# Kernel tuning notes

Hardware: AMD Instinct MI355X
Metric: run time of the kernel (lower is better)

## Reference

```python
import jax, jax.numpy as jnp
import numpy as np

QUANT_BLOCK = 32  # GGUF Q4_0-style block size
QUANT_ZERO = 8.0  # 4-bit codes are offset-binary around 8


def setup_inputs() -> dict:
    key = jax.random.key(0)
    k_x, k_q, k_s, k_up, k_dn, k_b = jax.random.split(key, 6)
    O, I, R = 4096, 4096, 16
    T = 2048  # tokens (batch*seq)
    x = jax.random.normal(k_x, (T, I), dtype=jnp.float32)
    # quantized 4-bit codes stored unpacked as int32 in [0, 16)
    q = jax.random.randint(k_q, (O, I), 0, 16, dtype=jnp.int32)
    # per-block scales (small positive, like real GGUF d values)
    scales = jax.random.uniform(k_s, (O, I // QUANT_BLOCK), dtype=jnp.float32) * 0.05
    lora_up = jax.random.normal(k_up, (O, R), dtype=jnp.float32) * 0.02
    lora_down = jax.random.normal(k_dn, (R, I), dtype=jnp.float32) * 0.02
    alpha = jnp.ones((), dtype=jnp.float32)
    bias = jax.random.normal(k_b, (O,), dtype=jnp.float32)
    return {"x": x, "q": q, "scales": scales, "lora_up": lora_up,
            "lora_down": lora_down, "alpha": alpha, "bias": bias}


def _dequant(q, scales):
    # q: [O, I] int codes; scales: [O, I/BLOCK] per-block scale
    O, I = q.shape
    qf = q.reshape(O, I // QUANT_BLOCK, QUANT_BLOCK).astype(scales.dtype)
    w = (qf - QUANT_ZERO) * scales[:, :, None]  # [O, I/B, B]
    return w.reshape(O, I)


def reference(x, q, scales, lora_up, lora_down, alpha, bias):
    # on-the-fly dequant (GGMLLayer.get_weight -> dequantize_tensor)
    W = _dequant(q, scales)  # [O, I]
    # LoRA patch apply (ray_calculate_weight): W += alpha * up @ down
    W = W + alpha * jnp.einsum('or,ri->oi', lora_up, lora_down)
    # linear forward: y = x @ W^T + b
    return jnp.einsum('ti,oi->to', x, W) + bias
```

## Files before the change

kernel.cpp:

```cpp
#include <hip/hip_runtime.h>
#include <hip/hip_bf16.h>
#include <stdint.h>

#define T_DIM 2048
#define I_DIM 4096
#define O_DIM 4096
#define R_DIM 16
#define QBLK  32

typedef __bf16 bf16x8 __attribute__((ext_vector_type(8)));
typedef float  floatx4 __attribute__((ext_vector_type(4)));
typedef unsigned short ushort_t;

#define AS1 __attribute__((address_space(1)))
#define AS3 __attribute__((address_space(3)))

__device__ __forceinline__ ushort_t f2bf(float f) {
  unsigned u = __float_as_uint(f);
  u += 0x7FFFu + ((u >> 16) & 1u);
  return (ushort_t)(u >> 16);
}

__device__ __forceinline__ float dot4(float4 a, float4 b) {
  return a.x * b.x + a.y * b.y + a.z * b.z + a.w * b.w;
}

__global__ __launch_bounds__(256) void k_prep(const float* __restrict__ x,
                                              const int* __restrict__ q,
                                              const float* __restrict__ scales,
                                              const float* __restrict__ down,
                                              const float* __restrict__ alphap,
                                              ushort_t* __restrict__ xb,
                                              ushort_t* __restrict__ wb,
                                              float* __restrict__ xd) {
  __shared__ float ds[16 * 512];
  const int b = blockIdx.x, tid = threadIdx.x;

  if (b < 4096) {
    int idx = b * 256 + tid;
    const float4* xp = (const float4*)x;
    float4 a = xp[idx * 2], c = xp[idx * 2 + 1];
    union { ushort_t u[8]; uint4 v; } r;
    r.u[0] = f2bf(a.x); r.u[1] = f2bf(a.y); r.u[2] = f2bf(a.z); r.u[3] = f2bf(a.w);
    r.u[4] = f2bf(c.x); r.u[5] = f2bf(c.y); r.u[6] = f2bf(c.z); r.u[7] = f2bf(c.w);
    ((uint4*)xb)[idx] = r.v;
    return;
  }
  if (b < 12288) {
    int idx = (b - 4096) * 256 + tid;
    int o  = idx >> 9;
    int i0 = (idx & 511) * 8;
    float s = scales[o * (I_DIM / QBLK) + (i0 >> 5)];
    const int4* qp = (const int4*)(q + (size_t)o * I_DIM + i0);
    int4 q0 = qp[0], q1 = qp[1];
    union { ushort_t u[8]; uint4 v; } r;
    r.u[0] = f2bf((float)(q0.x - 8) * s); r.u[1] = f2bf((float)(q0.y - 8) * s);
    r.u[2] = f2bf((float)(q0.z - 8) * s); r.u[3] = f2bf((float)(q0.w - 8) * s);
    r.u[4] = f2bf((float)(q1.x - 8) * s); r.u[5] = f2bf((float)(q1.y - 8) * s);
    r.u[6] = f2bf((float)(q1.z - 8) * s); r.u[7] = f2bf((float)(q1.w - 8) * s);
    ((uint4*)wb)[idx] = r.v;
    return;
  }
  {
    const int blk = b - 12288;
    const int tl = tid >> 5, s = tid & 31;
    const int t = blk * 8 + tl;
    float acc[16];
#pragma unroll
    for (int r = 0; r < 16; ++r) acc[r] = 0.f;
    for (int c = 0; c < 8; ++c) {
      const int ib = c * 512;
      __syncthreads();
#pragma unroll
      for (int j = 0; j < 8; ++j) {
        int e = j * 256 + tid;
        int r = e >> 7, col = e & 127;
        ((float4*)ds)[e] = ((const float4*)(down + (size_t)r * I_DIM + ib))[col];
      }
      __syncthreads();
#pragma unroll
      for (int j = 0; j < 4; ++j) {
        float4 xv = ((const float4*)(x + (size_t)t * I_DIM + ib))[s + 32 * j];
#pragma unroll
        for (int r = 0; r < 16; ++r) {
          float4 dv = ((const float4*)ds)[r * 128 + s + 32 * j];
          acc[r] += dot4(xv, dv);
        }
      }
    }
    const float al = alphap[0];
#pragma unroll
    for (int r = 0; r < 16; ++r) {
      float v = acc[r];
      v += __shfl_down(v, 16, 32);
      v += __shfl_down(v, 8, 32);
      v += __shfl_down(v, 4, 32);
      v += __shfl_down(v, 2, 32);
      v += __shfl_down(v, 1, 32);
      if (s == 0) xd[t * 16 + r] = v * al;
    }
  }
}


#define BK 32
#define NT (I_DIM / BK)
#define TILE_E (128 * BK)

__device__ __forceinline__ void stage2(const ushort_t* __restrict__ g,
                                       ushort_t* lds0, int wv, int lane) {
#pragma unroll
  for (int it = 0; it < 2; ++it) {
    const int seg_base = it * 256 + wv * 64;
    const int seg = seg_base + lane;
    const int r  = seg >> 2;
    const int cg = (seg & 3) ^ (r & 3);
    __builtin_amdgcn_global_load_lds(
        (const AS1 char*)(g + (size_t)r * I_DIM + cg * 8),
        (AS3 char*)(lds0 + seg_base * 8), 16, 0, 0);
  }
}

template<int VM, bool STG>
__device__ __forceinline__ void ktile(const ushort_t* __restrict__ Ac,
                                      const ushort_t* __restrict__ Bc,
                                      ushort_t* Ast, ushort_t* Bst,
                                      const ushort_t* ga, const ushort_t* gb,
                                      floatx4 (&acc)[4][4], int wv, int lane) {
  const int quad = lane >> 4, m16 = lane & 15;
  const int wm = wv >> 1, wn = wv & 1;
  bf16x8 af[4], bf0[2], bf1[2];

#pragma unroll
  for (int im = 0; im < 4; ++im) {
    const int m = wm * 64 + im * 16 + m16;
    af[im] = *(const bf16x8*)(Ac + (m * 4 + (quad ^ (m & 3))) * 8);
  }
#pragma unroll
  for (int in_ = 0; in_ < 2; ++in_) {
    const int n = wn * 64 + in_ * 16 + m16;
    bf0[in_] = *(const bf16x8*)(Bc + (n * 4 + (quad ^ (n & 3))) * 8);
  }
  if constexpr (STG) stage2(ga, Ast, wv, lane);
  __builtin_amdgcn_s_barrier();
  asm volatile("s_waitcnt lgkmcnt(0)" ::: "memory");
  __builtin_amdgcn_sched_barrier(0);
  __builtin_amdgcn_s_setprio(1);
#pragma unroll
  for (int im = 0; im < 4; ++im)
#pragma unroll
    for (int in_ = 0; in_ < 2; ++in_)
      acc[im][in_] = __builtin_amdgcn_mfma_f32_16x16x32_bf16(
          af[im], bf0[in_], acc[im][in_], 0, 0, 0);
  __builtin_amdgcn_s_setprio(0);
  __builtin_amdgcn_s_barrier();

#pragma unroll
  for (int in_ = 0; in_ < 2; ++in_) {
    const int n = wn * 64 + (in_ + 2) * 16 + m16;
    bf1[in_] = *(const bf16x8*)(Bc + (n * 4 + (quad ^ (n & 3))) * 8);
  }
  if constexpr (STG) stage2(gb, Bst, wv, lane);
  __builtin_amdgcn_s_barrier();
  asm volatile("s_waitcnt lgkmcnt(0)" ::: "memory");
  __builtin_amdgcn_sched_barrier(0);
  __builtin_amdgcn_s_setprio(1);
#pragma unroll
  for (int im = 0; im < 4; ++im)
#pragma unroll
    for (int in_ = 0; in_ < 2; ++in_)
      acc[im][in_ + 2] = __builtin_amdgcn_mfma_f32_16x16x32_bf16(
          af[im], bf1[in_], acc[im][in_ + 2], 0, 0, 0);
  __builtin_amdgcn_s_setprio(0);
  if constexpr (VM == 8)      asm volatile("s_waitcnt vmcnt(8)" ::: "memory");
  else if constexpr (VM == 4) asm volatile("s_waitcnt vmcnt(4)" ::: "memory");
  else if constexpr (VM == 0) asm volatile("s_waitcnt vmcnt(0)" ::: "memory");
  if constexpr (VM >= 0) __builtin_amdgcn_sched_barrier(0);
  __builtin_amdgcn_s_barrier();
}

__global__ __launch_bounds__(256, 2) void k_gemm(const ushort_t* __restrict__ xb,
                                                 const ushort_t* __restrict__ wb,
                                                 const float* __restrict__ bias,
                                                 const float* __restrict__ xd,
                                                 const float* __restrict__ up,
                                                 float* __restrict__ y) {
  __shared__ __align__(16) ushort_t As[4][TILE_E];
  __shared__ __align__(16) ushort_t Bs[4][TILE_E];

  const int tid = threadIdx.x;
  const int wv = tid >> 6, lane = tid & 63;

  const int id = blockIdx.x;
  const int sid = (id & 7) * 64 + (id >> 3);
  const int bx = sid >> 4;
  const int by = sid & 15;
  const int oT = bx * 128, tT = by * 128;

  const ushort_t* ap = xb + (size_t)tT * I_DIM;
  const ushort_t* bp = wb + (size_t)oT * I_DIM;

  floatx4 acc[4][4] = {};

#pragma unroll
  for (int t = 0; t < 3; ++t) {
    stage2(ap + t * BK, As[t], wv, lane);
    stage2(bp + t * BK, Bs[t], wv, lane);
  }
  asm volatile("s_waitcnt vmcnt(8)" ::: "memory");
  __builtin_amdgcn_sched_barrier(0);
  __builtin_amdgcn_s_barrier();

  for (int kt = 0; kt < NT - 3; ++kt) {
    const int cur = kt & 3, st = (kt + 3) & 3;
    ktile<8, true>(As[cur], Bs[cur], As[st], Bs[st],
                   ap + (size_t)(kt + 3) * BK, bp + (size_t)(kt + 3) * BK,
                   acc, wv, lane);
  }
  ktile<4, false>(As[(NT - 3) & 3], Bs[(NT - 3) & 3], nullptr, nullptr,
                  nullptr, nullptr, acc, wv, lane);
  ktile<0, false>(As[(NT - 2) & 3], Bs[(NT - 2) & 3], nullptr, nullptr,
                  nullptr, nullptr, acc, wv, lane);
  ktile<-1, false>(As[(NT - 1) & 3], Bs[(NT - 1) & 3], nullptr, nullptr,
                   nullptr, nullptr, acc, wv, lane);

  const int quad = lane >> 4, m16 = lane & 15;
  const int wm = wv >> 1, wn = wv & 1;
#pragma unroll
  for (int im = 0; im < 4; ++im) {
#pragma unroll
    for (int reg = 0; reg < 4; ++reg) {
      const int t = tT + wm * 64 + im * 16 + quad * 4 + reg;
      const float4* xr = (const float4*)(xd + t * 16);
      float4 x0 = xr[0], x1 = xr[1], x2 = xr[2], x3 = xr[3];
#pragma unroll
      for (int in_ = 0; in_ < 4; ++in_) {
        const int o = oT + wn * 64 + in_ * 16 + m16;
        const float4* ur = (const float4*)(up + (size_t)o * R_DIM);
        float lv = dot4(x0, ur[0]) + dot4(x1, ur[1]) +
                   dot4(x2, ur[2]) + dot4(x3, ur[3]);
        y[(size_t)t * O_DIM + o] = acc[im][in_][reg] + lv + bias[o];
      }
    }
  }
}

extern "C" void kernel_launch(void* const* d_in, const int* in_sizes, int n_in,
                              void* d_out, int out_size, void* d_ws, size_t ws_size,
                              hipStream_t stream) {
  const float* x      = (const float*)d_in[0];
  const int*   q      = (const int*)d_in[1];
  const float* scales = (const float*)d_in[2];
  const float* up     = (const float*)d_in[3];
  const float* down   = (const float*)d_in[4];
  const float* alpha  = (const float*)d_in[5];
  const float* bias   = (const float*)d_in[6];
  float* y = (float*)d_out;

  ushort_t* xb = (ushort_t*)d_ws;
  ushort_t* wb = (ushort_t*)((char*)d_ws + (size_t)T_DIM * I_DIM * 2);
  float*    xd = (float*)((char*)d_ws + (size_t)T_DIM * I_DIM * 2 + (size_t)O_DIM * I_DIM * 2);

  hipLaunchKernelGGL(k_prep, dim3(4096 + 8192 + 256), dim3(256), 0, stream,
                     x, q, scales, down, alpha, xb, wb, xd);
  hipLaunchKernelGGL(k_gemm, dim3((O_DIM / 128) * (T_DIM / 128)), dim3(256), 0, stream,
                     xb, wb, bias, xd, up, y);
}
```

Baseline: 457.0 us.

## Merge GEMM k-tile half-steps, change LDS swizzle, reorder prep block roles

The two half-phases of each k-tile are merged into one phase. All four B fragments are loaded up front and both A and B tiles are staged together, which halves the barriers per k-tile but uses more fragment registers. The LDS XOR swizzle now mixes r>>2 into the column group to cut bank conflicts, and fragments are read with inline-asm ds_read_b128 from raw LDS addresses. In the prep kernel, the slower LoRA-down reduction blocks move to the front of the grid so they are scheduled first.

```diff
diff --git a/kernel.cpp b/kernel.cpp
--- a/kernel.cpp
+++ b/kernel.cpp
@@ -36,8 +36,8 @@
   __shared__ float ds[16 * 512];
   const int b = blockIdx.x, tid = threadIdx.x;
 
-  if (b < 4096) {
-    int idx = b * 256 + tid;
+  if (b >= 256 && b < 4352) {
+    int idx = (b - 256) * 256 + tid;
     const float4* xp = (const float4*)x;
     float4 a = xp[idx * 2], c = xp[idx * 2 + 1];
     union { ushort_t u[8]; uint4 v; } r;
@@ -46,8 +46,8 @@
     ((uint4*)xb)[idx] = r.v;
     return;
   }
-  if (b < 12288) {
-    int idx = (b - 4096) * 256 + tid;
+  if (b >= 4352) {
+    int idx = (b - 4352) * 256 + tid;
     int o  = idx >> 9;
     int i0 = (idx & 511) * 8;
     float s = scales[o * (I_DIM / QBLK) + (i0 >> 5)];
@@ -62,7 +62,7 @@
     return;
   }
   {
-    const int blk = b - 12288;
+    const int blk = b;
     const int tl = tid >> 5, s = tid & 31;
     const int t = blk * 8 + tl;
     float acc[16];
@@ -107,6 +107,12 @@
 #define NT (I_DIM / BK)
 #define TILE_E (128 * BK)
 
+__device__ __forceinline__ bf16x8 lds_read16(unsigned addr) {
+  bf16x8 d;
+  asm volatile("ds_read_b128 %0, %1" : "=v"(d) : "v"(addr));
+  return d;
+}
+
 __device__ __forceinline__ void stage2(const ushort_t* __restrict__ g,
                                        ushort_t* lds0, int wv, int lane) {
 #pragma unroll
@@ -114,7 +120,7 @@
     const int seg_base = it * 256 + wv * 64;
     const int seg = seg_base + lane;
     const int r  = seg >> 2;
-    const int cg = (seg & 3) ^ (r & 3);
+    const int cg = (seg & 3) ^ ((r + (r >> 2)) & 3);
     __builtin_amdgcn_global_load_lds(
         (const AS1 char*)(g + (size_t)r * I_DIM + cg * 8),
         (AS3 char*)(lds0 + seg_base * 8), 16, 0, 0);
@@ -122,26 +128,24 @@
 }
 
 template<int VM, bool STG>
-__device__ __forceinline__ void ktile(const ushort_t* __restrict__ Ac,
-                                      const ushort_t* __restrict__ Bc,
+__device__ __forceinline__ void ktile(unsigned aB, unsigned bB,
                                       ushort_t* Ast, ushort_t* Bst,
                                       const ushort_t* ga, const ushort_t* gb,
                                       floatx4 (&acc)[4][4], int wv, int lane) {
   const int quad = lane >> 4, m16 = lane & 15;
   const int wm = wv >> 1, wn = wv & 1;
-  bf16x8 af[4], bf0[2], bf1[2];
-
+  bf16x8 af[4], bfr[4];
 #pragma unroll
   for (int im = 0; im < 4; ++im) {
     const int m = wm * 64 + im * 16 + m16;
-    af[im] = *(const bf16x8*)(Ac + (m * 4 + (quad ^ (m & 3))) * 8);
-  }
-#pragma unroll
-  for (int in_ = 0; in_ < 2; ++in_) {
+    af[im] = lds_read16(aB + (unsigned)(m * 64 + ((quad ^ ((m + (m >> 2)) & 3)) << 4)));
+  }
+#pragma unroll
+  for (int in_ = 0; in_ < 4; ++in_) {
     const int n = wn * 64 + in_ * 16 + m16;
-    bf0[in_] = *(const bf16x8*)(Bc + (n * 4 + (quad ^ (n & 3))) * 8);
-  }
-  if constexpr (STG) stage2(ga, Ast, wv, lane);
+    bfr[in_] = lds_read16(bB + (unsigned)(n * 64 + ((quad ^ ((n + (n >> 2)) & 3)) << 4)));
+  }
+  if constexpr (STG) { stage2(ga, Ast, wv, lane); stage2(gb, Bst, wv, lane); }
   __builtin_amdgcn_s_barrier();
   asm volatile("s_waitcnt lgkmcnt(0)" ::: "memory");
   __builtin_amdgcn_sched_barrier(0);
@@ -149,28 +153,9 @@
 #pragma unroll
   for (int im = 0; im < 4; ++im)
 #pragma unroll
-    for (int in_ = 0; in_ < 2; ++in_)
+    for (int in_ = 0; in_ < 4; ++in_)
       acc[im][in_] = __builtin_amdgcn_mfma_f32_16x16x32_bf16(
-          af[im], bf0[in_], acc[im][in_], 0, 0, 0);
-  __builtin_amdgcn_s_setprio(0);
-  __builtin_amdgcn_s_barrier();
-
-#pragma unroll
-  for (int in_ = 0; in_ < 2; ++in_) {
-    const int n = wn * 64 + (in_ + 2) * 16 + m16;
-    bf1[in_] = *(const bf16x8*)(Bc + (n * 4 + (quad ^ (n & 3))) * 8);
-  }
-  if constexpr (STG) stage2(gb, Bst, wv, lane);
-  __builtin_amdgcn_s_barrier();
-  asm volatile("s_waitcnt lgkmcnt(0)" ::: "memory");
-  __builtin_amdgcn_sched_barrier(0);
-  __builtin_amdgcn_s_setprio(1);
-#pragma unroll
-  for (int im = 0; im < 4; ++im)
-#pragma unroll
-    for (int in_ = 0; in_ < 2; ++in_)
-      acc[im][in_ + 2] = __builtin_amdgcn_mfma_f32_16x16x32_bf16(
-          af[im], bf1[in_], acc[im][in_ + 2], 0, 0, 0);
+          af[im], bfr[in_], acc[im][in_], 0, 0, 0);
   __builtin_amdgcn_s_setprio(0);
   if constexpr (VM == 8)      asm volatile("s_waitcnt vmcnt(8)" ::: "memory");
   else if constexpr (VM == 4) asm volatile("s_waitcnt vmcnt(4)" ::: "memory");
@@ -200,6 +185,9 @@
   const ushort_t* ap = xb + (size_t)tT * I_DIM;
   const ushort_t* bp = wb + (size_t)oT * I_DIM;
 
+  const unsigned asB = (unsigned)(uintptr_t)(AS3 ushort_t*)&As[0][0];
+  const unsigned bsB = (unsigned)(uintptr_t)(AS3 ushort_t*)&Bs[0][0];
+
   floatx4 acc[4][4] = {};
 
 #pragma unroll
@@ -213,16 +201,17 @@
 
   for (int kt = 0; kt < NT - 3; ++kt) {
     const int cur = kt & 3, st = (kt + 3) & 3;
-    ktile<8, true>(As[cur], Bs[cur], As[st], Bs[st],
+    ktile<8, true>(asB + cur * (TILE_E * 2), bsB + cur * (TILE_E * 2),
+                   As[st], Bs[st],
                    ap + (size_t)(kt + 3) * BK, bp + (size_t)(kt + 3) * BK,
                    acc, wv, lane);
   }
-  ktile<4, false>(As[(NT - 3) & 3], Bs[(NT - 3) & 3], nullptr, nullptr,
-                  nullptr, nullptr, acc, wv, lane);
-  ktile<0, false>(As[(NT - 2) & 3], Bs[(NT - 2) & 3], nullptr, nullptr,
-                  nullptr, nullptr, acc, wv, lane);
-  ktile<-1, false>(As[(NT - 1) & 3], Bs[(NT - 1) & 3], nullptr, nullptr,
-                   nullptr, nullptr, acc, wv, lane);
+  ktile<4, false>(asB + ((NT - 3) & 3) * (TILE_E * 2), bsB + ((NT - 3) & 3) * (TILE_E * 2),
+                  nullptr, nullptr, nullptr, nullptr, acc, wv, lane);
+  ktile<0, false>(asB + ((NT - 2) & 3) * (TILE_E * 2), bsB + ((NT - 2) & 3) * (TILE_E * 2),
+                  nullptr, nullptr, nullptr, nullptr, acc, wv, lane);
+  ktile<-1, false>(asB + ((NT - 1) & 3) * (TILE_E * 2), bsB + ((NT - 1) & 3) * (TILE_E * 2),
+                   nullptr, nullptr, nullptr, nullptr, acc, wv, lane);
 
   const int quad = lane >> 4, m16 = lane & 15;
   const int wm = wv >> 1, wn = wv & 1;
@@ -261,7 +250,7 @@
   ushort_t* wb = (ushort_t*)((char*)d_ws + (size_t)T_DIM * I_DIM * 2);
   float*    xd = (float*)((char*)d_ws + (size_t)T_DIM * I_DIM * 2 + (size_t)O_DIM * I_DIM * 2);
 
-  hipLaunchKernelGGL(k_prep, dim3(4096 + 8192 + 256), dim3(256), 0, stream,
+  hipLaunchKernelGGL(k_prep, dim3(256 + 4096 + 8192), dim3(256), 0, stream,
                      x, q, scales, down, alpha, xb, wb, xd);
   hipLaunchKernelGGL(k_gemm, dim3((O_DIM / 128) * (T_DIM / 128)), dim3(256), 0, stream,
                      xb, wb, bias, xd, up, y);
```

After: 454.1 us. No clear change (-0.6%).
